# Kernel optimization log

Measured on AMD Instinct MI355X. Metric: run time of the kernel, lower is better.

The kernel has to match this reference:

```python
import jax, jax.numpy as jnp
import numpy as np

TEMPERATURE = 0.5
N, K, L, D = 2048, 8, 64, 64


def setup_inputs() -> dict:
    key = jax.random.key(0)
    k1, k2, k3 = jax.random.split(key, 3)
    similarity_matrix = jax.random.normal(k1, (N, N), dtype=jnp.float32)
    batch_emb_om = jax.random.normal(k2, (N, L, D), dtype=jnp.float32)
    index = jax.random.randint(k3, (N, K), 0, N, dtype=jnp.int64)
    return {"similarity_matrix": similarity_matrix,
            "batch_emb_om": batch_emb_om,
            "index": index}


def reference(similarity_matrix, batch_emb_om, index):
    # divide=True path of AggregationRebuild
    sim = similarity_matrix / TEMPERATURE
    # gather each row's neighbor similarities: [N, K]
    sub_similarity = jnp.take_along_axis(sim, index, axis=1)
    rebuild_weight_matrix = jax.nn.softmax(sub_similarity, axis=-1)  # [N, K]
    # gather neighbor features: [N, K, L, D]
    neighbor_features = batch_emb_om[index]
    # softmax-weighted sum over neighbors -> [N, L, D]
    rebuild_oral_batch_emb = jnp.einsum('nk,nkld->nld',
                                        rebuild_weight_matrix, neighbor_features)
    return (rebuild_weight_matrix, rebuild_oral_batch_emb)
```

## Files before the change

kernel.cpp:

```cpp
#include <hip/hip_runtime.h>


constexpr int N = 2048;
constexpr int K = 8;
constexpr int L = 64;
constexpr int D = 64;
constexpr int LD = L * D;
constexpr float INV_TEMP = 2.0f;

__global__ __launch_bounds__(256) void agg_rebuild_kernel(
    const float* __restrict__ sim,
    const float* __restrict__ emb,
    const int*   __restrict__ idx32,
    float* __restrict__ w_out,
    float* __restrict__ rebuild) {
  const int n   = blockIdx.x;
  const int tid = threadIdx.x;

  __shared__ int   nb[K];
  __shared__ float sraw[K];
  __shared__ float wsm[K];
  __shared__ int   is64_s;

  if (tid == 0) {
    int acc = idx32[1] | idx32[3] | idx32[5] | idx32[7] |
              idx32[9] | idx32[11] | idx32[13] | idx32[15];
    is64_s = (acc == 0) ? 1 : 0;
  }
  __syncthreads();
  const bool is64 = (is64_s != 0);

  if (tid < K) {
    const int flat = n * K + tid;
    const int j = is64 ? idx32[2 * flat] : idx32[flat];
    nb[tid]   = j;
    sraw[tid] = sim[(size_t)n * N + j] * INV_TEMP;
  }
  __syncthreads();

  if (tid < K) {
    float m = sraw[0];
#pragma unroll
    for (int k = 1; k < K; ++k) m = fmaxf(m, sraw[k]);
    float sum = 0.0f;
#pragma unroll
    for (int k = 0; k < K; ++k) sum += expf(sraw[k] - m);
    const float wk = expf(sraw[tid] - m) / sum;
    wsm[tid] = wk;
    w_out[n * K + tid] = wk;
  }
  __syncthreads();

  float wr[K];
  const float4* __restrict__ erow[K];
#pragma unroll
  for (int k = 0; k < K; ++k) {
    wr[k]   = wsm[k];
    erow[k] = reinterpret_cast<const float4*>(emb + (size_t)nb[k] * LD);
  }
  float4* __restrict__ out4 = reinterpret_cast<float4*>(rebuild + (size_t)n * LD);

#pragma unroll
  for (int it = 0; it < LD / 4 / 256; ++it) {
    const int c = tid + it * 256;
    float4 acc = make_float4(0.f, 0.f, 0.f, 0.f);
#pragma unroll
    for (int k = 0; k < K; ++k) {
      const float4 v = erow[k][c];
      acc.x = fmaf(wr[k], v.x, acc.x);
      acc.y = fmaf(wr[k], v.y, acc.y);
      acc.z = fmaf(wr[k], v.z, acc.z);
      acc.w = fmaf(wr[k], v.w, acc.w);
    }
    out4[c] = acc;
  }
}

extern "C" void kernel_launch(void* const* d_in, const int* in_sizes, int n_in,
                              void* d_out, int out_size, void* d_ws, size_t ws_size,
                              hipStream_t stream) {
  const float* sim = (const float*)d_in[0];
  const float* emb = (const float*)d_in[1];
  const int*   idx = (const int*)d_in[2];
  float* out     = (float*)d_out;
  float* w_out   = out;
  float* rebuild = out + (size_t)N * K;

  hipLaunchKernelGGL(agg_rebuild_kernel, dim3(N), dim3(256), 0, stream,
                     sim, emb, idx, w_out, rebuild);
}
```

Baseline: 117.2 us.

## Split softmax weights into separate kernel and tile rebuild across rows

```diff
diff --git a/kernel.cpp b/kernel.cpp
--- a/kernel.cpp
+++ b/kernel.cpp
@@ -1,78 +1,95 @@
 #include <hip/hip_runtime.h>
 
 
-constexpr int N = 2048;
-constexpr int K = 8;
-constexpr int L = 64;
-constexpr int D = 64;
-constexpr int LD = L * D;
+typedef float f32x4 __attribute__((ext_vector_type(4)));
+
+constexpr int N  = 2048;
+constexpr int K  = 8;
+constexpr int LD = 64 * 64;
 constexpr float INV_TEMP = 2.0f;
 
-__global__ __launch_bounds__(256) void agg_rebuild_kernel(
+constexpr int TILE   = 512;
+constexpr int NTILES = LD / TILE;
+constexpr int RPB    = 8;
+
+__global__ __launch_bounds__(256) void weights_kernel(
     const float* __restrict__ sim,
-    const float* __restrict__ emb,
     const int*   __restrict__ idx32,
     float* __restrict__ w_out,
-    float* __restrict__ rebuild) {
-  const int n   = blockIdx.x;
-  const int tid = threadIdx.x;
+    float* __restrict__ w_ws,
+    int*   __restrict__ j_ws) {
+  const int g = blockIdx.x * 256 + threadIdx.x;
+  const int r = g >> 3;
+  const int k = g & 7;
 
-  __shared__ int   nb[K];
-  __shared__ float sraw[K];
-  __shared__ float wsm[K];
-  __shared__ int   is64_s;
-
-  if (tid == 0) {
+  __shared__ int is64_s;
+  if (threadIdx.x == 0) {
     int acc = idx32[1] | idx32[3] | idx32[5] | idx32[7] |
               idx32[9] | idx32[11] | idx32[13] | idx32[15];
     is64_s = (acc == 0) ? 1 : 0;
   }
   __syncthreads();
-  const bool is64 = (is64_s != 0);
 
-  if (tid < K) {
-    const int flat = n * K + tid;
-    const int j = is64 ? idx32[2 * flat] : idx32[flat];
-    nb[tid]   = j;
-    sraw[tid] = sim[(size_t)n * N + j] * INV_TEMP;
+  const int flat = r * K + k;
+  const int j = is64_s ? idx32[2 * flat] : idx32[flat];
+  const float s = sim[(size_t)r * N + j] * INV_TEMP;
+
+  float m = s;
+  m = fmaxf(m, __shfl_xor(m, 1, 8));
+  m = fmaxf(m, __shfl_xor(m, 2, 8));
+  m = fmaxf(m, __shfl_xor(m, 4, 8));
+  const float e = expf(s - m);
+  float sum = e;
+  sum += __shfl_xor(sum, 1, 8);
+  sum += __shfl_xor(sum, 2, 8);
+  sum += __shfl_xor(sum, 4, 8);
+  const float w = e / sum;
+
+  w_out[flat] = w;
+  w_ws[flat]  = w;
+  j_ws[flat]  = j;
+}
+
+__global__ __launch_bounds__(256) void rebuild_kernel(
+    const float* __restrict__ emb,
+    const float* __restrict__ w_ws,
+    const int*   __restrict__ j_ws,
+    float* __restrict__ rebuild) {
+  const int tile = blockIdx.x & (NTILES - 1);
+  const int rg   = blockIdx.x >> 3;
+  const int r0   = rg * RPB;
+  const int tid  = threadIdx.x;
+
+  __shared__ float w_lds[RPB][K];
+  __shared__ int   j_lds[RPB][K];
+  if (tid < RPB * K) {
+    w_lds[tid >> 3][tid & 7] = w_ws[r0 * K + tid];
+    j_lds[tid >> 3][tid & 7] = j_ws[r0 * K + tid];
   }
   __syncthreads();
 
-  if (tid < K) {
-    float m = sraw[0];
-#pragma unroll
-    for (int k = 1; k < K; ++k) m = fmaxf(m, sraw[k]);
-    float sum = 0.0f;
-#pragma unroll
-    for (int k = 0; k < K; ++k) sum += expf(sraw[k] - m);
-    const float wk = expf(sraw[tid] - m) / sum;
-    wsm[tid] = wk;
-    w_out[n * K + tid] = wk;
-  }
-  __syncthreads();
-
-  float wr[K];
-  const float4* __restrict__ erow[K];
-#pragma unroll
-  for (int k = 0; k < K; ++k) {
-    wr[k]   = wsm[k];
-    erow[k] = reinterpret_cast<const float4*>(emb + (size_t)nb[k] * LD);
-  }
-  float4* __restrict__ out4 = reinterpret_cast<float4*>(rebuild + (size_t)n * LD);
+  const int c   = tid & 127;
+  const int sub = tid >> 7;
+  const int col = tile * TILE + c * 4;
 
 #pragma unroll
-  for (int it = 0; it < LD / 4 / 256; ++it) {
-    const int c = tid + it * 256;
-    float4 acc = make_float4(0.f, 0.f, 0.f, 0.f);
+  for (int it = 0; it < RPB / 2; ++it) {
+    const int rl = it * 2 + sub;
+    float w[K];
+    const f32x4* p[K];
 #pragma unroll
     for (int k = 0; k < K; ++k) {
-      const float4 v = erow[k][c];
-      acc.x = fmaf(wr[k], v.x, acc.x);
-      acc.y = fmaf(wr[k], v.y, acc.y);
-      acc.z = fmaf(wr[k], v.z, acc.z);
-      acc.w = fmaf(wr[k], v.w, acc.w);
+      w[k] = w_lds[rl][k];
+      p[k] = reinterpret_cast<const f32x4*>(emb + (size_t)j_lds[rl][k] * LD + col);
     }
-    out4[c] = acc;
+    f32x4 acc = (f32x4)(0.0f);
+#pragma unroll
+    for (int k = 0; k < K; ++k) {
+      const f32x4 v = *p[k];
+      acc += w[k] * v;
+    }
+    f32x4* o = reinterpret_cast<f32x4*>(rebuild + (size_t)(r0 + rl) * LD + col);
+    __builtin_nontemporal_store(acc, o);
   }
 }
 
@@ -86,6 +103,11 @@
   float* w_out   = out;
   float* rebuild = out + (size_t)N * K;
 
-  hipLaunchKernelGGL(agg_rebuild_kernel, dim3(N), dim3(256), 0, stream,
-                     sim, emb, idx, w_out, rebuild);
+  float* w_ws = (float*)d_ws;
+  int*   j_ws = (int*)(w_ws + (size_t)N * K);
+
+  hipLaunchKernelGGL(weights_kernel, dim3(N * K / 256), dim3(256), 0, stream,
+                     sim, idx, w_out, w_ws, j_ws);
+  hipLaunchKernelGGL(rebuild_kernel, dim3((N / RPB) * NTILES), dim3(256), 0, stream,
+                     emb, w_ws, j_ws, rebuild);
 }
```

Result: faster. 99.97 us, median of 2 (-14.7%).
